# Performance work log

Hardware: AMD Instinct MI355X
Metric: run time of the kernel (lower is better)

The kernel has to match this reference:

```python
import jax, jax.numpy as jnp
import numpy as np

# Polynomial coefficients from the original module (hard-coded in forward).
P00, P10, P20, P30 = 0.0, 0.0, 0.0, 0.0      # identity-kernel branch (all zero)
P01, P11, P21 = -0.000287, 0.266, -0.1097    # learned-weight branch
STRIDE, PAD = 1, 1


def _conv(x, w):
    # NCHW input, OIHW kernel -> NCHW output. Equivalent to
    # unfold(x).T @ w.view(O,-1).T reshaped back, i.e. torch's im2col matmul.
    return jax.lax.conv_general_dilated(
        x, w,
        window_strides=(STRIDE, STRIDE),
        padding=[(PAD, PAD), (PAD, PAD)],
        dimension_numbers=('NCHW', 'OIHW', 'NCHW'))


def setup_inputs() -> dict:
    key = jax.random.key(0)
    k1, k2 = jax.random.split(key)
    img = jax.random.normal(k1, (16, 64, 128, 128), dtype=jnp.float32)
    # weights initialized N(0, 0.8) in the original module
    weights = jax.random.normal(k2, (64, 64, 3, 3), dtype=jnp.float32) * 0.8
    identity_kernel = jnp.ones((64, 64, 3, 3), dtype=jnp.float32)
    return {"img": img, "weights": weights, "identity_kernel": identity_kernel}


def reference(img, weights, identity_kernel):
    kh, kw = weights.shape[2], weights.shape[3]
    # Elementwise polynomial applied to the input, then contracted against
    # the (identity, learned) kernels. matmul-with-unfold == convolution,
    # so we express it as two convs instead of materializing im2col.
    poly_id = P00 + P10 * img + P20 * img**2 + P30 * img**3  # == zeros here
    poly_w = P01 + P11 * img + P21 * img**2
    out = _conv(poly_id, identity_kernel) + _conv(poly_w, weights)
    return out / (3 * kh * kw)
```

## Files before the change

kernel.cpp:

```cpp
#include <hip/hip_runtime.h>


typedef __bf16 bf16;
typedef __attribute__((ext_vector_type(8))) __bf16 bf16x8;
typedef __attribute__((ext_vector_type(16))) float f32x16;

static constexpr float A0 = -0.000287f / 27.0f;
static constexpr float A1 =  0.266f    / 27.0f;
static constexpr float A2 = -0.1097f   / 27.0f;

#define NN 16
#define CI 64
#define HH 128
#define WW 128
#define OO 64

__global__ void repack_w(const float* __restrict__ w, bf16* __restrict__ wrb) {
    int idx = blockIdx.x * 256 + threadIdx.x;
    if (idx >= 9 * 8 * 64 * 8) return;
    int cj    = idx & 7;
    int o     = (idx >> 3) & 63;
    int cc8   = (idx >> 9) & 7;
    int slice = idx >> 12;
    int ky = slice / 3, kx = slice - ky * 3;
    int c = cc8 * 8 + cj;
    wrb[idx] = (bf16)w[((o * CI + c) * 3 + ky) * 3 + kx];
}

__global__ __launch_bounds__(512, 4) void conv_mfma(const float* __restrict__ img,
                                                    const bf16* __restrict__ wrb,
                                                    float* __restrict__ out) {
    __shared__ __align__(16) char smem[49920];
    bf16*  ilds = (bf16*)smem;
    float* elds = (float*)smem;

    const int tid = threadIdx.x;
    const int b   = blockIdx.x;
    const int y0  = (b & 31) * 4;
    const int n   = b >> 5;

    const int wv   = tid >> 6;
    const int lane = tid & 63;
    const int lm   = lane & 31;
    const int half = lane >> 5;
    const int yl   = wv >> 1;
    const int Xh   = (wv & 1) * 64;

    auto stage = [&](int chunk, int buf) {
        const int cbase = chunk * 16;
        bf16* dst = ilds + buf * 12480;
        for (int t = tid; t < 780; t += 512) {
            int r   = t / 130;
            int rem = t - r * 130;
            int ccl = rem / 65;
            int xh  = rem - ccl * 65;
            int yi  = y0 - 1 + r;
            bf16* rowp = dst + (r * 2 + ccl) * (130 * 8);
            if (xh < 64) {
                bf16x8 pk0, pk1;
                if ((unsigned)yi < 128u) {
                    const float* p = img + ((n * CI + cbase + ccl * 8) * HH + yi) * WW + 2 * xh;
                    #pragma unroll
                    for (int j = 0; j < 8; ++j) {
                        float2 v = *(const float2*)(p + j * HH * WW);
                        pk0[j] = (bf16)(A0 + v.x * (A1 + A2 * v.x));
                        pk1[j] = (bf16)(A0 + v.y * (A1 + A2 * v.y));
                    }
                } else {
                    #pragma unroll
                    for (int j = 0; j < 8; ++j) { pk0[j] = (bf16)0.0f; pk1[j] = (bf16)0.0f; }
                }
                *(bf16x8*)(rowp + (2 * xh + 1) * 8) = pk0;
                *(bf16x8*)(rowp + (2 * xh + 2) * 8) = pk1;
            } else {
                bf16x8 z;
                #pragma unroll
                for (int j = 0; j < 8; ++j) z[j] = (bf16)0.0f;
                *(bf16x8*)(rowp + 0) = z;
                *(bf16x8*)(rowp + 129 * 8) = z;
            }
        }
    };

    f32x16 acc[2][2];
    #pragma unroll
    for (int i = 0; i < 2; ++i)
        #pragma unroll
        for (int j = 0; j < 2; ++j)
            #pragma unroll
            for (int k = 0; k < 16; ++k) acc[i][j][k] = 0.0f;

    const bf16x8* wfr = (const bf16x8*)wrb;

    stage(0, 0);

    for (int chunk = 0; chunk < 4; ++chunk) {
        __syncthreads();
        if (chunk < 3) stage(chunk + 1, (chunk + 1) & 1);
        const bf16x8* ifr = (const bf16x8*)(ilds + (chunk & 1) * 12480);
        const int cc8g = chunk * 2 + half;
        #pragma unroll
        for (int ky = 0; ky < 3; ++ky) {
            const int r = yl + ky;
            #pragma unroll
            for (int kx = 0; kx < 3; ++kx) {
                const int slice = ky * 3 + kx;
                bf16x8 a0 = wfr[(slice * 8 + cc8g) * 64 + lm];
                bf16x8 a1 = wfr[(slice * 8 + cc8g) * 64 + 32 + lm];
                const int ib = (r * 2 + half) * 130 + Xh + lm + kx;
                bf16x8 b0 = ifr[ib];
                bf16x8 b1 = ifr[ib + 32];
                acc[0][0] = __builtin_amdgcn_mfma_f32_32x32x16_bf16(a0, b0, acc[0][0], 0, 0, 0);
                acc[0][1] = __builtin_amdgcn_mfma_f32_32x32x16_bf16(a0, b1, acc[0][1], 0, 0, 0);
                acc[1][0] = __builtin_amdgcn_mfma_f32_32x32x16_bf16(a1, b0, acc[1][0], 0, 0, 0);
                acc[1][1] = __builtin_amdgcn_mfma_f32_32x32x16_bf16(a1, b1, acc[1][1], 0, 0, 0);
            }
        }
    }

    #pragma unroll
    for (int p = 0; p < 4; ++p) {
        const int ot  = p >> 1;
        const int sub = p & 1;
        __syncthreads();
        #pragma unroll
        for (int xt = 0; xt < 2; ++xt) {
            const int x = Xh + xt * 32 + lm;
            #pragma unroll
            for (int q = 0; q < 2; ++q) {
                #pragma unroll
                for (int rb = 0; rb < 4; ++rb) {
                    const int rg  = (sub * 2 + q) * 4 + rb;
                    const int o16 = rb + 8 * q + 4 * half;
                    elds[(o16 * 4 + yl) * 128 + x] = acc[ot][xt][rg];
                }
            }
        }
        __syncthreads();
        #pragma unroll
        for (int j = 0; j < 4; ++j) {
            const int idx = tid + j * 512;
            const int x4  = idx & 31;
            const int yy  = (idx >> 5) & 3;
            const int o16 = idx >> 7;
            float4 v = ((const float4*)elds)[idx];
            float* dstp = out + ((n * OO + p * 16 + o16) * HH + (y0 + yy)) * WW + x4 * 4;
            *(float4*)dstp = v;
        }
    }
}

extern "C" void kernel_launch(void* const* d_in, const int* in_sizes, int n_in,
                              void* d_out, int out_size, void* d_ws, size_t ws_size,
                              hipStream_t stream) {
    const float* img = (const float*)d_in[0];
    const float* w   = (const float*)d_in[1];
    float* out = (float*)d_out;
    bf16* wrb  = (bf16*)d_ws;

    repack_w<<<(9 * 8 * 64 * 8 + 255) / 256, 256, 0, stream>>>(w, wrb);
    conv_mfma<<<NN * (HH / 4), 512, 0, stream>>>(img, wrb, out);
}
```

Baseline: 129.6 us.

## Halve conv tile to 2 rows and software-pipeline global loads into registers

Each block now covers 2 output rows with 256 threads instead of 4 rows with 512, which doubles the grid and shrinks LDS per block. Staging becomes a fixed per-thread mapping that issues float4 global loads for the next channel chunk into registers before the MFMA work on the current chunk. The values are converted and written to LDS afterwards, so global memory latency overlaps with compute. The trade-offs are more halo re-reads (4 input rows per 2 output rows instead of 6 per 4), extra registers to hold the prefetch, and a changed occupancy hint.

```diff
diff --git a/kernel.cpp b/kernel.cpp
--- a/kernel.cpp
+++ b/kernel.cpp
@@ -14,6 +14,7 @@
 #define HH 128
 #define WW 128
 #define OO 64
+#define HW (HH * WW)
 
 __global__ void repack_w(const float* __restrict__ w, bf16* __restrict__ wrb) {
     int idx = blockIdx.x * 256 + threadIdx.x;
@@ -27,17 +28,16 @@
     wrb[idx] = (bf16)w[((o * CI + c) * 3 + ky) * 3 + kx];
 }
 
-__global__ __launch_bounds__(512, 4) void conv_mfma(const float* __restrict__ img,
+__global__ __launch_bounds__(256, 3) void conv_mfma(const float* __restrict__ img,
                                                     const bf16* __restrict__ wrb,
                                                     float* __restrict__ out) {
-    __shared__ __align__(16) char smem[49920];
-    bf16*  ilds = (bf16*)smem;
-    float* elds = (float*)smem;
+    __shared__ __align__(16) bf16 ilds[2 * 4 * 2 * 130 * 8];
+    float* elds = (float*)ilds;
 
     const int tid = threadIdx.x;
     const int b   = blockIdx.x;
-    const int y0  = (b & 31) * 4;
-    const int n   = b >> 5;
+    const int y0  = (b & 63) * 2;
+    const int n   = b >> 6;
 
     const int wv   = tid >> 6;
     const int lane = tid & 63;
@@ -46,40 +46,51 @@
     const int yl   = wv >> 1;
     const int Xh   = (wv & 1) * 64;
 
-    auto stage = [&](int chunk, int buf) {
-        const int cbase = chunk * 16;
-        bf16* dst = ilds + buf * 12480;
-        for (int t = tid; t < 780; t += 512) {
-            int r   = t / 130;
-            int rem = t - r * 130;
-            int ccl = rem / 65;
-            int xh  = rem - ccl * 65;
-            int yi  = y0 - 1 + r;
-            bf16* rowp = dst + (r * 2 + ccl) * (130 * 8);
-            if (xh < 64) {
-                bf16x8 pk0, pk1;
-                if ((unsigned)yi < 128u) {
-                    const float* p = img + ((n * CI + cbase + ccl * 8) * HH + yi) * WW + 2 * xh;
-                    #pragma unroll
-                    for (int j = 0; j < 8; ++j) {
-                        float2 v = *(const float2*)(p + j * HH * WW);
-                        pk0[j] = (bf16)(A0 + v.x * (A1 + A2 * v.x));
-                        pk1[j] = (bf16)(A0 + v.y * (A1 + A2 * v.y));
-                    }
-                } else {
-                    #pragma unroll
-                    for (int j = 0; j < 8; ++j) { pk0[j] = (bf16)0.0f; pk1[j] = (bf16)0.0f; }
+    const int sxq  = tid & 31;
+    const int sccl = (tid >> 5) & 1;
+    const int sr   = tid >> 6;
+    const int syi  = y0 - 1 + sr;
+    const bool sval = (unsigned)syi < 128u;
+    const float* sbase = img + ((n * CI + sccl * 8) * HH + (sval ? syi : 0)) * WW + 4 * sxq;
+    bf16* srow = ilds + (sr * 2 + sccl) * (130 * 8) + (4 * sxq + 1) * 8;
+
+    if (tid < 32) {
+        const int bufi = tid & 1;
+        const int col  = (tid >> 1) & 1;
+        const int rc   = tid >> 2;
+        bf16x8 z;
+        #pragma unroll
+        for (int j = 0; j < 8; ++j) z[j] = (bf16)0.0f;
+        *(bf16x8*)(ilds + bufi * 8320 + rc * (130 * 8) + (col ? 129 * 8 : 0)) = z;
+    }
+
+    float4 pre[8];
+    auto issue = [&](int chunk) {
+        if (sval) {
+            const float* p = sbase + chunk * 16 * HW;
+            #pragma unroll
+            for (int j = 0; j < 8; ++j) pre[j] = *(const float4*)(p + j * HW);
+        }
+    };
+    auto commit = [&](int buf) {
+        bf16x8 pk[4];
+        if (sval) {
+            #pragma unroll
+            for (int x4 = 0; x4 < 4; ++x4)
+                #pragma unroll
+                for (int j = 0; j < 8; ++j) {
+                    float v = ((const float*)&pre[j])[x4];
+                    pk[x4][j] = (bf16)(A0 + v * (A1 + A2 * v));
                 }
-                *(bf16x8*)(rowp + (2 * xh + 1) * 8) = pk0;
-                *(bf16x8*)(rowp + (2 * xh + 2) * 8) = pk1;
-            } else {
-                bf16x8 z;
+        } else {
+            #pragma unroll
+            for (int x4 = 0; x4 < 4; ++x4)
                 #pragma unroll
-                for (int j = 0; j < 8; ++j) z[j] = (bf16)0.0f;
-                *(bf16x8*)(rowp + 0) = z;
-                *(bf16x8*)(rowp + 129 * 8) = z;
-            }
+                for (int j = 0; j < 8; ++j) pk[x4][j] = (bf16)0.0f;
         }
+        bf16* dst = srow + buf * 8320;
+        #pragma unroll
+        for (int x4 = 0; x4 < 4; ++x4) *(bf16x8*)(dst + x4 * 8) = pk[x4];
     };
 
     f32x16 acc[2][2];
@@ -92,12 +103,8 @@
 
     const bf16x8* wfr = (const bf16x8*)wrb;
 
-    stage(0, 0);
-
-    for (int chunk = 0; chunk < 4; ++chunk) {
-        __syncthreads();
-        if (chunk < 3) stage(chunk + 1, (chunk + 1) & 1);
-        const bf16x8* ifr = (const bf16x8*)(ilds + (chunk & 1) * 12480);
+    auto compute = [&](int chunk) {
+        const bf16x8* ifr = (const bf16x8*)(ilds + (chunk & 1) * 8320);
         const int cc8g = chunk * 2 + half;
         #pragma unroll
         for (int ky = 0; ky < 3; ++ky) {
@@ -116,7 +123,17 @@
                 acc[1][1] = __builtin_amdgcn_mfma_f32_32x32x16_bf16(a1, b1, acc[1][1], 0, 0, 0);
             }
         }
+    };
+
+    issue(0);
+    #pragma unroll
+    for (int chunk = 0; chunk < 4; ++chunk) {
+        if (chunk > 0) compute(chunk - 1);
+        commit(chunk & 1);
+        if (chunk < 3) issue(chunk + 1);
+        __syncthreads();
     }
+    compute(3);
 
     #pragma unroll
     for (int p = 0; p < 4; ++p) {
@@ -127,25 +144,23 @@
         for (int xt = 0; xt < 2; ++xt) {
             const int x = Xh + xt * 32 + lm;
             #pragma unroll
-            for (int q = 0; q < 2; ++q) {
+            for (int q = 0; q < 2; ++q)
                 #pragma unroll
                 for (int rb = 0; rb < 4; ++rb) {
                     const int rg  = (sub * 2 + q) * 4 + rb;
                     const int o16 = rb + 8 * q + 4 * half;
-                    elds[(o16 * 4 + yl) * 128 + x] = acc[ot][xt][rg];
+                    elds[(o16 * 2 + yl) * 128 + x] = acc[ot][xt][rg];
                 }
-            }
         }
         __syncthreads();
         #pragma unroll
         for (int j = 0; j < 4; ++j) {
-            const int idx = tid + j * 512;
+            const int idx = tid + j * 256;
             const int x4  = idx & 31;
-            const int yy  = (idx >> 5) & 3;
-            const int o16 = idx >> 7;
+            const int y2  = (idx >> 5) & 1;
+            const int o16 = idx >> 6;
             float4 v = ((const float4*)elds)[idx];
-            float* dstp = out + ((n * OO + p * 16 + o16) * HH + (y0 + yy)) * WW + x4 * 4;
-            *(float4*)dstp = v;
+            *(float4*)(out + ((n * OO + p * 16 + o16) * HH + (y0 + y2)) * WW + 4 * x4) = v;
         }
     }
 }
@@ -159,5 +174,5 @@
     bf16* wrb  = (bf16*)d_ws;
 
     repack_w<<<(9 * 8 * 64 * 8 + 255) / 256, 256, 0, stream>>>(w, wrb);
-    conv_mfma<<<NN * (HH / 4), 512, 0, stream>>>(img, wrb, out);
+    conv_mfma<<<NN * (HH / 2), 256, 0, stream>>>(img, wrb, out);
 }
```

After: 148.0 us. +14.2%, slower.
